# Kernel tuning notes

Measured on AMD Instinct MI355X. Metric: run time of the kernel, lower is better.

Reference implementation:

```python
import jax, jax.numpy as jnp
import numpy as np

DIM = 4096
N_HEADS = 32
N_KV_HEADS = 8
HEAD_DIM = DIM // N_HEADS  # 128
N_REP = N_HEADS // N_KV_HEADS  # 4
FFN_HIDDEN = 11008
EPS = 1e-6
B, S = 4, 2048


def rms_norm(x, gamma):
    # x: [b, s, d]
    var = jnp.mean(x * x, axis=-1, keepdims=True)
    return gamma * (x * jax.lax.rsqrt(var + EPS))


def apply_rope(x, cos, sin):
    # x: [b, s, h, d]; cos/sin: [s, d/2]. Complex rotation on (even, odd) pairs.
    x2 = x.reshape(*x.shape[:-1], HEAD_DIM // 2, 2)
    x0, x1 = x2[..., 0], x2[..., 1]
    c = cos[None, :, None, :]
    s = sin[None, :, None, :]
    r0 = x0 * c - x1 * s
    r1 = x0 * s + x1 * c
    return jnp.stack([r0, r1], axis=-1).reshape(x.shape)


def setup_inputs() -> dict:
    key = jax.random.key(0)
    ks = jax.random.split(key, 16)
    sc = 0.02
    inp = {
        "x": jax.random.normal(ks[0], (B, S, DIM), dtype=jnp.float32),
        "freqs": jax.random.uniform(ks[1], (S, HEAD_DIM // 2), dtype=jnp.float32) * (2 * np.pi),
        "start_pos": 0,
        "gamma_attn": jnp.ones((DIM,), jnp.float32),
        "gamma_ffn": jnp.ones((DIM,), jnp.float32),
        "wq_w": sc * jax.random.normal(ks[2], (N_HEADS * HEAD_DIM, DIM), jnp.float32),
        "wq_b": jnp.zeros((N_HEADS * HEAD_DIM,), jnp.float32),
        "wk_w": sc * jax.random.normal(ks[3], (N_KV_HEADS * HEAD_DIM, DIM), jnp.float32),
        "wk_b": jnp.zeros((N_KV_HEADS * HEAD_DIM,), jnp.float32),
        "wv_w": sc * jax.random.normal(ks[4], (N_KV_HEADS * HEAD_DIM, DIM), jnp.float32),
        "wv_b": jnp.zeros((N_KV_HEADS * HEAD_DIM,), jnp.float32),
        "wo_w": sc * jax.random.normal(ks[5], (DIM, N_HEADS * HEAD_DIM), jnp.float32),
        "wo_b": jnp.zeros((DIM,), jnp.float32),
        "w1_w": sc * jax.random.normal(ks[6], (FFN_HIDDEN, DIM), jnp.float32),
        "w3_w": sc * jax.random.normal(ks[7], (FFN_HIDDEN, DIM), jnp.float32),
        "w2_w": sc * jax.random.normal(ks[8], (DIM, FFN_HIDDEN), jnp.float32),
    }
    return inp


def reference(x, freqs, start_pos, gamma_attn, gamma_ffn,
              wq_w, wq_b, wk_w, wk_b, wv_w, wv_b, wo_w, wo_b,
              w1_w, w3_w, w2_w):
    cos, sin = jnp.cos(freqs), jnp.sin(freqs)

    # --- attention sublayer ---
    xn = rms_norm(x, gamma_attn)
    xq = (xn @ wq_w.T + wq_b).reshape(B, S, N_HEADS, HEAD_DIM)
    xk = (xn @ wk_w.T + wk_b).reshape(B, S, N_KV_HEADS, HEAD_DIM)
    xv = (xn @ wv_w.T + wv_b).reshape(B, S, N_KV_HEADS, HEAD_DIM)
    xq = apply_rope(xq, cos, sin)
    xk = apply_rope(xk, cos, sin)

    # KV cache: start_pos=0 prefill -> cache slice [0:start_pos+S] == current xk/xv
    keys = jnp.repeat(xk, N_REP, axis=2)   # [b, s, n_heads, d]
    values = jnp.repeat(xv, N_REP, axis=2)

    scores = jnp.einsum('bqhd,bkhd->bhqk', xq, keys) / np.sqrt(HEAD_DIM)
    probs = jax.nn.softmax(scores.astype(jnp.float32), axis=-1).astype(xq.dtype)
    attn = jnp.einsum('bhqk,bkhd->bqhd', probs, values).reshape(B, S, DIM)
    h = x + attn @ wo_w.T + wo_b

    # --- FFN sublayer (LLaMA SwiGLU) ---
    hn = rms_norm(h, gamma_ffn)
    ff = (jax.nn.silu(hn @ w1_w.T) * (hn @ w3_w.T)) @ w2_w.T
    return h + ff
```

## Files before the change

kernel.cpp:

```cpp
#include <hip/hip_runtime.h>
#include <hip/hip_bf16.h>

#define DIM   4096
#define NH    32
#define NKV   8
#define HD    128
#define FFNH  11008
#define BATCH 4
#define SEQ   2048
#define MTOT  (BATCH*SEQ)

using bf16x8_t = __attribute__((ext_vector_type(8))) short;
using f32x4_t  = __attribute__((ext_vector_type(4))) float;

typedef const __attribute__((address_space(1))) unsigned int GlbU32;
typedef __attribute__((address_space(3))) unsigned int LdsU32;

__device__ __forceinline__ unsigned short f2b(float f) {
  union { float f; unsigned int u; } v; v.f = f;
  return (unsigned short)((v.u + 0x7fffu + ((v.u >> 16) & 1u)) >> 16);
}
__device__ __forceinline__ float b2f(unsigned short b) {
  union { unsigned int u; float f; } v; v.u = ((unsigned int)b) << 16;
  return v.f;
}
__device__ __forceinline__ void gll16(const void* g, void* l) {
  __builtin_amdgcn_global_load_lds((GlbU32*)g, (LdsU32*)l, 16, 0, 0);
}

#define VM8  asm volatile("s_waitcnt vmcnt(8)" ::: "memory")
#define VM4M asm volatile("s_waitcnt vmcnt(4)" ::: "memory")
#define VM0  asm volatile("s_waitcnt vmcnt(0)" ::: "memory")

__global__ __launch_bounds__(256)
void cvt_bf16_k(const float* __restrict__ src, unsigned short* __restrict__ dst)
{
  const size_t i = ((size_t)blockIdx.x * 256 + threadIdx.x) * 8;
  const float4 a = *(const float4*)&src[i];
  const float4 b = *(const float4*)&src[i + 4];
  union { int4 v; unsigned short u[8]; } o;
  o.u[0] = f2b(a.x); o.u[1] = f2b(a.y); o.u[2] = f2b(a.z); o.u[3] = f2b(a.w);
  o.u[4] = f2b(b.x); o.u[5] = f2b(b.y); o.u[6] = f2b(b.z); o.u[7] = f2b(b.w);
  *(int4*)&dst[i] = o.v;
}

__global__ __launch_bounds__(256)
void rmsnorm_k(const float* __restrict__ X, const float* __restrict__ gamma,
               unsigned short* __restrict__ Y)
{
  const int row = blockIdx.x, t = threadIdx.x;
  const float* xr = X + (size_t)row * DIM;
  float4 v[4];
  float ss = 0.f;
#pragma unroll
  for (int p = 0; p < 4; ++p) {
    v[p] = *(const float4*)&xr[p * 1024 + t * 4];
    ss += v[p].x*v[p].x + v[p].y*v[p].y + v[p].z*v[p].z + v[p].w*v[p].w;
  }
#pragma unroll
  for (int off = 32; off >= 1; off >>= 1) ss += __shfl_xor(ss, off, 64);
  __shared__ float red[4];
  if ((t & 63) == 0) red[t >> 6] = ss;
  __syncthreads();
  const float tot = red[0] + red[1] + red[2] + red[3];
  const float rn = rsqrtf(tot * (1.f / DIM) + 1e-6f);
  unsigned short* yr = Y + (size_t)row * DIM;
#pragma unroll
  for (int p = 0; p < 4; ++p) {
    const float4 gv = *(const float4*)&gamma[p * 1024 + t * 4];
    short4 o;
    o.x = (short)f2b(v[p].x * gv.x * rn);
    o.y = (short)f2b(v[p].y * gv.y * rn);
    o.z = (short)f2b(v[p].z * gv.z * rn);
    o.w = (short)f2b(v[p].w * gv.w * rn);
    *(short4*)&yr[p * 1024 + t * 4] = o;
  }
}

template<int NHT>
__global__ __launch_bounds__(256)
void rope_k(unsigned short* __restrict__ buf, const float* __restrict__ fr)
{
  const int u = blockIdx.x * 256 + threadIdx.x;
  const int per_row = NHT * 16;
  const int row  = u / per_row;
  const int rem  = u - row * per_row;
  const int head = rem >> 4;
  const int i4   = (rem & 15) << 2;
  const int s    = row & (SEQ - 1);
  unsigned short* p = buf + (size_t)row * (NHT * HD) + head * HD + i4 * 2;
  union { int4 v; unsigned short u16[8]; } d;
  d.v = *(const int4*)p;
  const float4 f = *(const float4*)&fr[s * 64 + i4];
  const float fa[4] = {f.x, f.y, f.z, f.w};
#pragma unroll
  for (int i = 0; i < 4; ++i) {
    float sn, c;
    __sincosf(fa[i], &sn, &c);
    const float x0 = b2f(d.u16[2*i]), x1 = b2f(d.u16[2*i+1]);
    d.u16[2*i]   = f2b(x0 * c - x1 * sn);
    d.u16[2*i+1] = f2b(x0 * sn + x1 * c);
  }
  *(int4*)p = d.v;
}

template<int MODE>
__global__ __launch_bounds__(512)
void gemm256(const unsigned short* __restrict__ A,
             const unsigned short* __restrict__ W,
             const unsigned short* __restrict__ W3p,
             const float* __restrict__ bias,
             const float* res,
             float* outF,
             unsigned short* __restrict__ outH,
             const unsigned short* __restrict__ wkp,
             const unsigned short* __restrict__ wvp,
             const float* __restrict__ bkp,
             const float* __restrict__ bvp,
             unsigned short* __restrict__ okp,
             unsigned short* __restrict__ ovp,
             int K)
{
  __shared__ __align__(16) char smem[131072];
  const int t = threadIdx.x, lane = t & 63, wid = t >> 6;
  const int wr = wid >> 2, wc = wid & 3;
  const int G = gridDim.x, bid = blockIdx.x;
  const int wg = (bid & 7) * (G >> 3) + (bid >> 3);
  const int NBN = G >> 5;
  const int span = NBN << 3;
  const int tmg = wg / span, rr = wg - tmg * span;
  const int tn = rr >> 3, tm = (tmg << 3) + (rr & 7);
  const int m0 = tm << 8;
  const int NSUB = K >> 5;

  const unsigned short *P1, *P2;
  const float* bp = bias;
  unsigned short* oh = outH;
  int nloc = 0, colsN = 4096;
  if constexpr (MODE == 0) {
    const int n0 = tn << 8;
    if (n0 < 4096)      { nloc = n0;        P1 = W   + (size_t)nloc * K; bp = bias; oh = outH; colsN = 4096; }
    else if (n0 < 5120) { nloc = n0 - 4096; P1 = wkp + (size_t)nloc * K; bp = bkp;  oh = okp;  colsN = 1024; }
    else                { nloc = n0 - 5120; P1 = wvp + (size_t)nloc * K; bp = bvp;  oh = ovp;  colsN = 1024; }
    P2 = P1 + (size_t)128 * K;
  } else if constexpr (MODE == 3) {
    const int n0w = tn << 7;
    P1 = W   + (size_t)n0w * K;
    P2 = W3p + (size_t)n0w * K;
    nloc = n0w;
  } else {
    const int n0 = tn << 8;
    P1 = W + (size_t)n0 * K;
    P2 = P1 + (size_t)128 * K;
    nloc = n0;
  }

  const int r0 = t >> 2, gg = t & 3;
  const int gsw = gg ^ ((r0 >> 1) & 3);

  auto stA = [&](int sig) {
    if (sig < NSUB) {
      const int slot = sig & 3;
      gll16(A + (size_t)(m0 + r0) * K + sig * 32 + gsw * 8,
            smem + slot * 16384 + wid * 1024);
      gll16(A + (size_t)(m0 + 128 + r0) * K + sig * 32 + gsw * 8,
            smem + slot * 16384 + 8192 + wid * 1024);
    }
  };
  auto stB = [&](int sig) {
    if (sig < NSUB) {
      const int slot = sig & 3;
      gll16(P1 + (size_t)r0 * K + sig * 32 + gsw * 8,
            smem + 65536 + slot * 16384 + wid * 1024);
      gll16(P2 + (size_t)r0 * K + sig * 32 + gsw * 8,
            smem + 65536 + slot * 16384 + 8192 + wid * 1024);
    }
  };
  auto rdA = [&](int slot, int mo) -> bf16x8_t {
    const int lrow = wr * 128 + mo + (lane & 15);
    const int g = (lane >> 4) ^ ((lrow >> 1) & 3);
    return *(const bf16x8_t*)(smem + slot * 16384 + lrow * 64 + g * 16);
  };
  auto rdB = [&](int slot, int nf) -> bf16x8_t {
    const int brow = wc * 64 + nf * 16 + (lane & 15);
    const int g = (lane >> 4) ^ ((brow >> 1) & 3);
    return *(const bf16x8_t*)(smem + 65536 + slot * 16384 + brow * 64 + g * 16);
  };

  f32x4_t acc[8][4];
#pragma unroll
  for (int i = 0; i < 8; ++i)
#pragma unroll
    for (int j = 0; j < 4; ++j) acc[i][j] = (f32x4_t)0.f;

  stA(0); stB(0); stA(1); stB(1); stA(2); stB(2);
  VM8;
  __builtin_amdgcn_s_barrier();

  for (int p = 0; p < NSUB; ++p) {
    const int slot = p & 3;
    bf16x8_t bfv[4], afv[8];
#pragma unroll
    for (int n = 0; n < 4; ++n) bfv[n] = rdB(slot, n);
#pragma unroll
    for (int m = 0; m < 8; ++m) afv[m] = rdA(slot, m * 16);
    stA(p + 3); stB(p + 3);
    __builtin_amdgcn_s_setprio(1);
#pragma unroll
    for (int m = 0; m < 8; ++m)
#pragma unroll
      for (int n = 0; n < 4; ++n)
        acc[m][n] = __builtin_amdgcn_mfma_f32_16x16x32_bf16(afv[m], bfv[n], acc[m][n], 0, 0, 0);
    __builtin_amdgcn_s_setprio(0);
    if (p < NSUB - 3)      { VM8; }
    else if (p == NSUB - 3){ VM4M; }
    else                   { VM0; }
    __builtin_amdgcn_s_barrier();
  }

  if constexpr (MODE == 0) {
#pragma unroll
    for (int ni = 0; ni < 4; ++ni) {
      const int col = nloc + wc * 64 + ni * 16 + (lane & 15);
      const float bv = bp[col];
#pragma unroll
      for (int mi = 0; mi < 8; ++mi)
#pragma unroll
        for (int r = 0; r < 4; ++r) {
          const int row = m0 + wr * 128 + mi * 16 + (lane >> 4) * 4 + r;
          oh[(size_t)row * colsN + col] = f2b(acc[mi][ni][r] + bv);
        }
    }
  } else if constexpr (MODE == 1 || MODE == 2) {
#pragma unroll
    for (int ni = 0; ni < 4; ++ni) {
      const int col = nloc + wc * 64 + ni * 16 + (lane & 15);
      float bv = 0.f;
      if constexpr (MODE == 1) bv = bias[col];
#pragma unroll
      for (int mi = 0; mi < 8; ++mi)
#pragma unroll
        for (int r = 0; r < 4; ++r) {
          const int row = m0 + wr * 128 + mi * 16 + (lane >> 4) * 4 + r;
          const size_t idx = (size_t)row * 4096 + col;
          outF[idx] = acc[mi][ni][r] + bv + res[idx];
        }
    }
  } else {
    if (wc >= 2) {
      const int widx = wr * 2 + (wc - 2);
#pragma unroll
      for (int ni = 0; ni < 4; ++ni)
#pragma unroll
        for (int mi = 0; mi < 8; ++mi)
#pragma unroll
          for (int r = 0; r < 4; ++r) {
            const int lrow = mi * 16 + (lane >> 4) * 4 + r;
            const int ncol = ni * 16 + (lane & 15);
            *(unsigned short*)(smem + widx * 16384 + lrow * 128 + ncol * 2) =
                f2b(acc[mi][ni][r]);
          }
    }
    __syncthreads();
    if (wc < 2) {
      const int widx = wr * 2 + wc;
#pragma unroll
      for (int ni = 0; ni < 4; ++ni)
#pragma unroll
        for (int mi = 0; mi < 8; ++mi)
#pragma unroll
          for (int r = 0; r < 4; ++r) {
            const int lrow = mi * 16 + (lane >> 4) * 4 + r;
            const int ncol = ni * 16 + (lane & 15);
            const float s3 = b2f(*(const unsigned short*)(smem + widx * 16384 + lrow * 128 + ncol * 2));
            const float s1 = acc[mi][ni][r];
            const float sig = 1.f / (1.f + __expf(-s1));
            const int row = m0 + wr * 128 + lrow;
            outH[(size_t)row * FFNH + nloc + wc * 64 + ncol] = f2b(s1 * sig * s3);
          }
    }
  }
}

__global__ __launch_bounds__(256)
void attn_k(const unsigned short* __restrict__ Q, const unsigned short* __restrict__ Kb,
            const unsigned short* __restrict__ Vb, unsigned short* __restrict__ O)
{
  __shared__ unsigned short Qs[8192];
  __shared__ unsigned short Ks[4][4096];
  __shared__ unsigned short Vt[2][4096];
  __shared__ unsigned short Ps[4096];
  const int t = threadIdx.x, lane = t & 63, wid = t >> 6;
  const int bx = blockIdx.x;
  const int qt = bx & 31, h = (bx >> 5) & 31, b = bx >> 10;
  const int kvh = h >> 2;
  const float rs = 0.08838834764831845f;
  constexpr int NPAIR = SEQ / 64;

#pragma unroll
  for (int oo = 0; oo < 4; ++oo) {
    const int o = wid * 4 + oo;
    const int row = o * 4 + (lane >> 4);
    const int gl  = (lane & 15) ^ (row & 7);
    gll16(Q + (size_t)(b * SEQ + qt * 64 + row) * DIM + h * HD + gl * 8, &Qs[o * 512]);
  }

  const unsigned short* Kbase = Kb + (size_t)(b * SEQ) * (NKV * HD) + kvh * HD;
  const unsigned short* Vbase = Vb + (size_t)(b * SEQ) * (NKV * HD) + kvh * HD;

  auto stK = [&](int kt, int slot) {
#pragma unroll
    for (int oo = 0; oo < 2; ++oo) {
      const int o = wid * 2 + oo;
      const int row = o * 4 + (lane >> 4);
      const int gl  = (lane & 15) ^ (row & 7);
      gll16(Kbase + (size_t)(kt * 32 + row) * (NKV * HD) + gl * 8, &Ks[slot][o * 512]);
    }
  };
  const int kv = t >> 3, dc = (t & 7) << 4;
  const int colv = kv ^ ((t & 3) << 3);
  auto ldV = [&](int kt, int4& lo, int4& hi) {
    const unsigned short* gp = Vbase + (size_t)(kt * 32 + kv) * (NKV * HD) + dc;
    lo = *(const int4*)gp;
    hi = *(const int4*)(gp + 8);
  };
  auto wrV = [&](int slot, int4 vlo, int4 vhi) {
    union { int4 v; unsigned short u[8]; } lo, hi;
    lo.v = vlo; hi.v = vhi;
#pragma unroll
    for (int j = 0; j < 8; ++j) Vt[slot][(dc + j) * 32 + colv] = lo.u[j];
#pragma unroll
    for (int j = 0; j < 8; ++j) Vt[slot][(dc + 8 + j) * 32 + colv] = hi.u[j];
  };

  int4 a0l, a0h, a1l, a1h, b0l, b0h, b1l, b1h;
  stK(0, 0); ldV(0, a0l, a0h); stK(1, 1); ldV(1, a1l, a1h);
  stK(2, 2); ldV(2, b0l, b0h); stK(3, 3); ldV(3, b1l, b1h);

  f32x4_t oa[8];
#pragma unroll
  for (int i = 0; i < 8; ++i) oa[i] = (f32x4_t)0.f;
  float mrun = -1e30f, lrun = 0.f;
  const int q0 = wid * 16;
  const int qc = lane & 15;
  const int psw = (qc & 7) << 3;

  auto pairIter = [&](int p, int sb, int4& l0, int4& h0, int4& l1, int4& h1) {
    if (p == NPAIR - 1) { VM0; } else { VM8; }
    wrV(0, l0, h0);
    wrV(1, l1, h1);
    asm volatile("s_waitcnt lgkmcnt(0)" ::: "memory");
    __builtin_amdgcn_s_barrier();

    f32x4_t st[4];
    st[0] = (f32x4_t)0.f; st[1] = (f32x4_t)0.f;
    st[2] = (f32x4_t)0.f; st[3] = (f32x4_t)0.f;
    const int arow = q0 + qc;
    const int kr0 = qc, kr1 = 16 + qc;
    __builtin_amdgcn_s_setprio(1);
#pragma unroll
    for (int ks = 0; ks < 4; ++ks) {
      const bf16x8_t aq  = *(const bf16x8_t*)&Qs[(arow * 128 + ks * 32 + (lane >> 4) * 8) ^ ((arow & 7) << 3)];
      const bf16x8_t k00 = *(const bf16x8_t*)&Ks[sb][(kr0 * 128 + ks * 32 + (lane >> 4) * 8) ^ ((kr0 & 7) << 3)];
      st[0] = __builtin_amdgcn_mfma_f32_16x16x32_bf16(k00, aq, st[0], 0, 0, 0);
      const bf16x8_t k01 = *(const bf16x8_t*)&Ks[sb][(kr1 * 128 + ks * 32 + (lane >> 4) * 8) ^ ((kr1 & 7) << 3)];
      st[1] = __builtin_amdgcn_mfma_f32_16x16x32_bf16(k01, aq, st[1], 0, 0, 0);
      const bf16x8_t k10 = *(const bf16x8_t*)&Ks[sb + 1][(kr0 * 128 + ks * 32 + (lane >> 4) * 8) ^ ((kr0 & 7) << 3)];
      st[2] = __builtin_amdgcn_mfma_f32_16x16x32_bf16(k10, aq, st[2], 0, 0, 0);
      const bf16x8_t k11 = *(const bf16x8_t*)&Ks[sb + 1][(kr1 * 128 + ks * 32 + (lane >> 4) * 8) ^ ((kr1 & 7) << 3)];
      st[3] = __builtin_amdgcn_mfma_f32_16x16x32_bf16(k11, aq, st[3], 0, 0, 0);
    }
    __builtin_amdgcn_s_setprio(0);

    float mx01 = fmaxf(fmaxf(st[0][0], st[0][1]), fmaxf(st[0][2], st[0][3]));
    float mx23 = fmaxf(fmaxf(st[1][0], st[1][1]), fmaxf(st[1][2], st[1][3]));
    float mx45 = fmaxf(fmaxf(st[2][0], st[2][1]), fmaxf(st[2][2], st[2][3]));
    float mx67 = fmaxf(fmaxf(st[3][0], st[3][1]), fmaxf(st[3][2], st[3][3]));
    float pm = fmaxf(fmaxf(mx01, mx23), fmaxf(mx45, mx67)) * rs;
    pm = fmaxf(pm, __shfl_xor(pm, 16, 64));
    pm = fmaxf(pm, __shfl_xor(pm, 32, 64));

    const int grow = __any(pm > mrun);
    if (grow) {
      const float mnew = fmaxf(mrun, pm);
      const float corr = __expf(mrun - mnew);
      mrun = mnew;
      lrun *= corr;
      float c4[4];
#pragma unroll
      for (int r = 0; r < 4; ++r) c4[r] = __shfl(corr, (lane >> 4) * 4 + r, 16);
#pragma unroll
      for (int i = 0; i < 8; ++i)
#pragma unroll
        for (int r = 0; r < 4; ++r) oa[i][r] *= c4[r];
    }

    float pv[4][4];
    float ssum = 0.f;
#pragma unroll
    for (int tt = 0; tt < 4; ++tt)
#pragma unroll
      for (int r = 0; r < 4; ++r) {
        pv[tt][r] = __expf(st[tt][r] * rs - mrun);
        ssum += pv[tt][r];
      }
    ssum += __shfl_xor(ssum, 16, 64);
    ssum += __shfl_xor(ssum, 32, 64);
    lrun += ssum;

#pragma unroll
    for (int tt = 0; tt < 4; ++tt)
#pragma unroll
      for (int r = 0; r < 4; ++r) {
        const int kvi = tt * 16 + (lane >> 4) * 4 + r;
        Ps[wid * 1024 + qc * 64 + (kvi ^ psw)] = f2b(pv[tt][r]);
      }
    const bf16x8_t pa0 = *(const bf16x8_t*)&Ps[wid * 1024 + qc * 64 + (((lane >> 4) * 8) ^ psw)];
    const bf16x8_t pa1 = *(const bf16x8_t*)&Ps[wid * 1024 + qc * 64 + ((32 + (lane >> 4) * 8) ^ psw)];

    __builtin_amdgcn_s_setprio(1);
#pragma unroll
    for (int nt2 = 0; nt2 < 8; ++nt2) {
      const bf16x8_t vf0 = *(const bf16x8_t*)&Vt[0][(nt2 * 16 + (lane & 15)) * 32 + (((lane >> 4) ^ (nt2 & 3)) << 3)];
      oa[nt2] = __builtin_amdgcn_mfma_f32_16x16x32_bf16(pa0, vf0, oa[nt2], 0, 0, 0);
      const bf16x8_t vf1 = *(const bf16x8_t*)&Vt[1][(nt2 * 16 + (lane & 15)) * 32 + (((lane >> 4) ^ (nt2 & 3)) << 3)];
      oa[nt2] = __builtin_amdgcn_mfma_f32_16x16x32_bf16(pa1, vf1, oa[nt2], 0, 0, 0);
    }
    __builtin_amdgcn_s_setprio(0);
    __builtin_amdgcn_s_barrier();
    if (p + 2 < NPAIR) {
      stK(2 * p + 4, sb);     ldV(2 * p + 4, l0, h0);
      stK(2 * p + 5, sb + 1); ldV(2 * p + 5, l1, h1);
    }
  };

  for (int j = 0; j < NPAIR / 2; ++j) {
    pairIter(2 * j,     0, a0l, a0h, a1l, a1h);
    pairIter(2 * j + 1, 2, b0l, b0h, b1l, b1h);
  }

  float inv[4];
#pragma unroll
  for (int r = 0; r < 4; ++r) inv[r] = 1.f / __shfl(lrun, (lane >> 4) * 4 + r, 16);
#pragma unroll
  for (int nt2 = 0; nt2 < 8; ++nt2) {
    const int col = h * HD + nt2 * 16 + (lane & 15);
#pragma unroll
    for (int r = 0; r < 4; ++r) {
      const int row = qt * 64 + q0 + (lane >> 4) * 4 + r;
      O[(size_t)(b * SEQ + row) * DIM + col] = f2b(oa[nt2][r] * inv[r]);
    }
  }
}

extern "C" void kernel_launch(void* const* d_in, const int* in_sizes, int n_in,
                              void* d_out, int out_size, void* d_ws, size_t ws_size,
                              hipStream_t stream)
{
  (void)in_sizes; (void)n_in; (void)out_size; (void)ws_size;
  const float* x   = (const float*)d_in[0];
  const float* fr  = (const float*)d_in[1];
  const float* ga  = (const float*)d_in[3];
  const float* gf  = (const float*)d_in[4];
  const float* wq  = (const float*)d_in[5];
  const float* wqb = (const float*)d_in[6];
  const float* wk  = (const float*)d_in[7];
  const float* wkb = (const float*)d_in[8];
  const float* wv  = (const float*)d_in[9];
  const float* wvb = (const float*)d_in[10];
  const float* wo  = (const float*)d_in[11];
  const float* wob = (const float*)d_in[12];
  const float* w1  = (const float*)d_in[13];
  const float* w3  = (const float*)d_in[14];
  const float* w2  = (const float*)d_in[15];
  float* out = (float*)d_out;

  constexpr size_t MB = 1ull << 20;
  char* ws = (char*)d_ws;
  unsigned short* xn = (unsigned short*)(ws);
  unsigned short* qb = (unsigned short*)(ws + 64*MB);
  unsigned short* kb = (unsigned short*)(ws + 128*MB);
  unsigned short* vb = (unsigned short*)(ws + 144*MB);
  unsigned short* ao = (unsigned short*)(ws + 160*MB);
  unsigned short* hn = (unsigned short*)(ws + 224*MB);
  unsigned short* g  = (unsigned short*)(ws);
  unsigned short* wscr = (unsigned short*)(ws + 288*MB);
  unsigned short* wqB = wscr;
  unsigned short* wkB = wscr + 16*MB;
  unsigned short* wvB = wscr + 20*MB;
  unsigned short* woB = wscr;
  unsigned short* w1B = wscr;
  unsigned short* w3B = wscr + 45*MB;
  unsigned short* w2B = wscr;

  rmsnorm_k<<<MTOT, 256, 0, stream>>>(x, ga, xn);
  cvt_bf16_k<<<(NH*HD*DIM)/2048,  256, 0, stream>>>(wq, wqB);
  cvt_bf16_k<<<(NKV*HD*DIM)/2048, 256, 0, stream>>>(wk, wkB);
  cvt_bf16_k<<<(NKV*HD*DIM)/2048, 256, 0, stream>>>(wv, wvB);
  gemm256<0><<<(MTOT/256)*((DIM+2*NKV*HD)/256), 512, 0, stream>>>(
      xn, wqB, nullptr, wqb, nullptr, nullptr, qb,
      wkB, wvB, wkb, wvb, kb, vb, DIM);
  rope_k<NH><<<(MTOT*NH*16)/256,  256, 0, stream>>>(qb, fr);
  rope_k<NKV><<<(MTOT*NKV*16)/256,256, 0, stream>>>(kb, fr);
  attn_k<<<BATCH*NH*(SEQ/64), 256, 0, stream>>>(qb, kb, vb, ao);
  cvt_bf16_k<<<(DIM*DIM)/2048, 256, 0, stream>>>(wo, woB);
  gemm256<1><<<(MTOT/256)*(DIM/256), 512, 0, stream>>>(
      ao, woB, nullptr, wob, x, out, nullptr,
      nullptr, nullptr, nullptr, nullptr, nullptr, nullptr, DIM);
  rmsnorm_k<<<MTOT, 256, 0, stream>>>(out, gf, hn);
  cvt_bf16_k<<<(FFNH*DIM)/2048, 256, 0, stream>>>(w1, w1B);
  cvt_bf16_k<<<(FFNH*DIM)/2048, 256, 0, stream>>>(w3, w3B);
  gemm256<3><<<(MTOT/256)*(FFNH/128), 512, 0, stream>>>(
      hn, w1B, w3B, nullptr, nullptr, nullptr, g,
      nullptr, nullptr, nullptr, nullptr, nullptr, nullptr, DIM);
  cvt_bf16_k<<<(FFNH*DIM)/2048, 256, 0, stream>>>(w2, w2B);
  gemm256<2><<<(MTOT/256)*(DIM/256), 512, 0, stream>>>(
      g, w2B, nullptr, nullptr, out, out, nullptr,
      nullptr, nullptr, nullptr, nullptr, nullptr, nullptr, FFNH);
}
```

Measured before the change: 3.647 ms.

## Keep Q fragments in registers and shrink attention LDS for higher occupancy

```diff
diff --git a/kernel.cpp b/kernel.cpp
--- a/kernel.cpp
+++ b/kernel.cpp
@@ -282,14 +282,13 @@
   }
 }
 
-__global__ __launch_bounds__(256)
+__global__ __launch_bounds__(256, 3)
 void attn_k(const unsigned short* __restrict__ Q, const unsigned short* __restrict__ Kb,
             const unsigned short* __restrict__ Vb, unsigned short* __restrict__ O)
 {
-  __shared__ unsigned short Qs[8192];
   __shared__ unsigned short Ks[4][4096];
   __shared__ unsigned short Vt[2][4096];
-  __shared__ unsigned short Ps[4096];
+  __shared__ unsigned short Ps[2560];
   const int t = threadIdx.x, lane = t & 63, wid = t >> 6;
   const int bx = blockIdx.x;
   const int qt = bx & 31, h = (bx >> 5) & 31, b = bx >> 10;
@@ -297,12 +296,15 @@
   const float rs = 0.08838834764831845f;
   constexpr int NPAIR = SEQ / 64;
 
-#pragma unroll
-  for (int oo = 0; oo < 4; ++oo) {
-    const int o = wid * 4 + oo;
-    const int row = o * 4 + (lane >> 4);
-    const int gl  = (lane & 15) ^ (row & 7);
-    gll16(Q + (size_t)(b * SEQ + qt * 64 + row) * DIM + h * HD + gl * 8, &Qs[o * 512]);
+  const int q0 = wid * 16;
+  const int qc = lane & 15;
+
+  bf16x8_t qf[4];
+  {
+    const unsigned short* qrow = Q + (size_t)(b * SEQ + qt * 64 + q0 + qc) * DIM
+                                   + h * HD + (lane >> 4) * 8;
+#pragma unroll
+    for (int ks = 0; ks < 4; ++ks) qf[ks] = *(const bf16x8_t*)(qrow + ks * 32);
   }
 
   const unsigned short* Kbase = Kb + (size_t)(b * SEQ) * (NKV * HD) + kvh * HD;
@@ -341,9 +343,12 @@
 #pragma unroll
   for (int i = 0; i < 8; ++i) oa[i] = (f32x4_t)0.f;
   float mrun = -1e30f, lrun = 0.f;
-  const int q0 = wid * 16;
-  const int qc = lane & 15;
-  const int psw = (qc & 7) << 3;
+  const int pbase = wid * 640 + qc * 40;
+  const int pwr   = pbase + (lane >> 4) * 4;
+
+  auto pack2 = [&](float x, float y) -> unsigned int {
+    return (unsigned int)f2b(x) | ((unsigned int)f2b(y) << 16);
+  };
 
   auto pairIter = [&](int p, int sb, int4& l0, int4& h0, int4& l1, int4& h1) {
     if (p == NPAIR - 1) { VM0; } else { VM8; }
@@ -355,20 +360,18 @@
     f32x4_t st[4];
     st[0] = (f32x4_t)0.f; st[1] = (f32x4_t)0.f;
     st[2] = (f32x4_t)0.f; st[3] = (f32x4_t)0.f;
-    const int arow = q0 + qc;
     const int kr0 = qc, kr1 = 16 + qc;
     __builtin_amdgcn_s_setprio(1);
 #pragma unroll
     for (int ks = 0; ks < 4; ++ks) {
-      const bf16x8_t aq  = *(const bf16x8_t*)&Qs[(arow * 128 + ks * 32 + (lane >> 4) * 8) ^ ((arow & 7) << 3)];
       const bf16x8_t k00 = *(const bf16x8_t*)&Ks[sb][(kr0 * 128 + ks * 32 + (lane >> 4) * 8) ^ ((kr0 & 7) << 3)];
-      st[0] = __builtin_amdgcn_mfma_f32_16x16x32_bf16(k00, aq, st[0], 0, 0, 0);
+      st[0] = __builtin_amdgcn_mfma_f32_16x16x32_bf16(k00, qf[ks], st[0], 0, 0, 0);
       const bf16x8_t k01 = *(const bf16x8_t*)&Ks[sb][(kr1 * 128 + ks * 32 + (lane >> 4) * 8) ^ ((kr1 & 7) << 3)];
-      st[1] = __builtin_amdgcn_mfma_f32_16x16x32_bf16(k01, aq, st[1], 0, 0, 0);
+      st[1] = __builtin_amdgcn_mfma_f32_16x16x32_bf16(k01, qf[ks], st[1], 0, 0, 0);
       const bf16x8_t k10 = *(const bf16x8_t*)&Ks[sb + 1][(kr0 * 128 + ks * 32 + (lane >> 4) * 8) ^ ((kr0 & 7) << 3)];
-      st[2] = __builtin_amdgcn_mfma_f32_16x16x32_bf16(k10, aq, st[2], 0, 0, 0);
+      st[2] = __builtin_amdgcn_mfma_f32_16x16x32_bf16(k10, qf[ks], st[2], 0, 0, 0);
       const bf16x8_t k11 = *(const bf16x8_t*)&Ks[sb + 1][(kr1 * 128 + ks * 32 + (lane >> 4) * 8) ^ ((kr1 & 7) << 3)];
-      st[3] = __builtin_amdgcn_mfma_f32_16x16x32_bf16(k11, aq, st[3], 0, 0, 0);
+      st[3] = __builtin_amdgcn_mfma_f32_16x16x32_bf16(k11, qf[ks], st[3], 0, 0, 0);
     }
     __builtin_amdgcn_s_setprio(0);
 
@@ -395,28 +398,29 @@
         for (int r = 0; r < 4; ++r) oa[i][r] *= c4[r];
     }
 
-    float pv[4][4];
     float ssum = 0.f;
 #pragma unroll
     for (int tt = 0; tt < 4; ++tt)
 #pragma unroll
       for (int r = 0; r < 4; ++r) {
-        pv[tt][r] = __expf(st[tt][r] * rs - mrun);
-        ssum += pv[tt][r];
+        st[tt][r] = __expf(st[tt][r] * rs - mrun);
+        ssum += st[tt][r];
       }
     ssum += __shfl_xor(ssum, 16, 64);
     ssum += __shfl_xor(ssum, 32, 64);
     lrun += ssum;
 
-#pragma unroll
-    for (int tt = 0; tt < 4; ++tt)
-#pragma unroll
-      for (int r = 0; r < 4; ++r) {
-        const int kvi = tt * 16 + (lane >> 4) * 4 + r;
-        Ps[wid * 1024 + qc * 64 + (kvi ^ psw)] = f2b(pv[tt][r]);
-      }
-    const bf16x8_t pa0 = *(const bf16x8_t*)&Ps[wid * 1024 + qc * 64 + (((lane >> 4) * 8) ^ psw)];
-    const bf16x8_t pa1 = *(const bf16x8_t*)&Ps[wid * 1024 + qc * 64 + ((32 + (lane >> 4) * 8) ^ psw)];
+    *(unsigned int*)&Ps[pwr]      = pack2(st[0][0], st[0][1]);
+    *(unsigned int*)&Ps[pwr + 2]  = pack2(st[0][2], st[0][3]);
+    *(unsigned int*)&Ps[pwr + 16] = pack2(st[1][0], st[1][1]);
+    *(unsigned int*)&Ps[pwr + 18] = pack2(st[1][2], st[1][3]);
+    const bf16x8_t pa0 = *(const bf16x8_t*)&Ps[pbase + (lane >> 4) * 8];
+    asm volatile("s_waitcnt lgkmcnt(0)" ::: "memory");
+    *(unsigned int*)&Ps[pwr]      = pack2(st[2][0], st[2][1]);
+    *(unsigned int*)&Ps[pwr + 2]  = pack2(st[2][2], st[2][3]);
+    *(unsigned int*)&Ps[pwr + 16] = pack2(st[3][0], st[3][1]);
+    *(unsigned int*)&Ps[pwr + 18] = pack2(st[3][2], st[3][3]);
+    const bf16x8_t pa1 = *(const bf16x8_t*)&Ps[pbase + (lane >> 4) * 8];
 
     __builtin_amdgcn_s_setprio(1);
 #pragma unroll
```

After: 3.631 ms. No clear change (-0.5%).
